# Optimization experiments

Measured on AMD Instinct MI355X. Metric: run time of the kernel, lower is better.

The kernel has to match this reference:

```python
import jax, jax.numpy as jnp
import numpy as np
from math import sqrt

B = 128        # graphs
P = 256        # nodes per graph
N = B * P      # total nodes
E = 524288     # edges (avg degree 16)
S = 32         # seed queries per graph
DQ = DK = DV = 128
H = 4          # heads


def setup_inputs() -> dict:
    key = jax.random.key(0)
    ks = jax.random.split(key, 10)
    Q = jax.random.normal(ks[0], (B, S, DQ), dtype=jnp.float32)
    x = jax.random.normal(ks[1], (N, DK), dtype=jnp.float32)
    # edges constrained within each graph block of P nodes
    src = jax.random.randint(ks[2], (E,), 0, N)
    dst = (src // P) * P + jax.random.randint(ks[3], (E,), 0, P)
    edge_index = jnp.stack([src, dst]).astype(jnp.int64)
    batch = (jnp.arange(N) // P).astype(jnp.int64)
    s = 1.0 / sqrt(DV)
    Wq = jax.random.normal(ks[4], (DQ, DV), dtype=jnp.float32) * s
    Wk = jax.random.normal(ks[5], (DK, DV), dtype=jnp.float32) * s
    Wv = jax.random.normal(ks[6], (DK, DV), dtype=jnp.float32) * s
    Wo = jax.random.normal(ks[7], (DV, DV), dtype=jnp.float32) * s
    z = jnp.zeros((DV,), jnp.float32)
    o = jnp.ones((DV,), jnp.float32)
    return {"Q": Q, "x": x, "edge_index": edge_index, "batch": batch,
            "Wq": Wq, "bq": z, "Wk": Wk, "bk": z, "Wv": Wv, "bv": z,
            "Wo": Wo, "bo": z, "g0": o, "b0": z, "g1": o, "b1": z}


def _gcn(x, edge_index, W, b):
    # PyG GCNConv: self-loops + symmetric deg^-1/2 normalization, then scatter-add
    xw = x @ W                                   # [N, DV]
    row, col = edge_index[0], edge_index[1]
    deg = jnp.zeros((N,), xw.dtype).at[col].add(1.0) + 1.0  # +1 for self-loop
    dinv = jax.lax.rsqrt(deg)
    coef = dinv[row] * dinv[col]                 # [E]
    out = jnp.zeros_like(xw).at[col].add(xw[row] * coef[:, None])
    out = out + xw * (dinv * dinv)[:, None]      # self-loop messages
    return out + b


def _ln(x, g, b, eps=1e-5):
    mu = x.mean(-1, keepdims=True)
    var = ((x - mu) ** 2).mean(-1, keepdims=True)
    return (x - mu) * jax.lax.rsqrt(var + eps) * g + b


def reference(Q, x, edge_index, batch, Wq, bq, Wk, bk, Wv, bv, Wo, bo, g0, b0, g1, b1):
    dh = DV // H
    Qp = Q @ Wq + bq                             # [B, S, DV]
    K = _gcn(x, edge_index, Wk, bk)              # [N, DV]
    V = _gcn(x, edge_index, Wv, bv)
    # to_dense_batch: equal-size graphs -> static reshape; mask all valid
    Kd = K.reshape(B, P, DV)
    Vd = V.reshape(B, P, DV)
    mask = jnp.ones((B, P), Qp.dtype)
    mask_add = (1.0 - mask) * -1e9               # [B, P]
    # split heads on last dim (== torch split(dim=2) + cat(dim=0))
    Qh = Qp.reshape(B, S, H, dh)
    Kh = Kd.reshape(B, P, H, dh)
    Vh = Vd.reshape(B, P, H, dh)
    scores = jnp.einsum('bshd,bphd->bhsp', Qh, Kh) / sqrt(DV)
    A = jax.nn.softmax(scores + mask_add[:, None, None, :], axis=-1)
    Oh = Qh + jnp.einsum('bhsp,bphd->bshd', A, Vh)
    O = Oh.reshape(B, S, DV)
    O = _ln(O, g0, b0)
    O = O + jax.nn.relu(O @ Wo + bo)
    O = _ln(O, g1, b1)
    return O
```

## Files before the change

### kernel.cpp

```cpp
#include <hip/hip_runtime.h>

typedef unsigned int uint32;
typedef unsigned short ushort;
typedef __attribute__((ext_vector_type(8))) short short8;
typedef __attribute__((ext_vector_type(4))) float f32x4;

#define NNODES 32768
#define NGRAPH 128
#define PNODES 256
#define SQ 32
#define NEDGE 524288
#define DIM 128
#define NHEAD 4
#define MAXDEG 64

__device__ __forceinline__ float u2f(uint32 u){ union{uint32 i; float f;} c; c.i=u; return c.f; }
__device__ __forceinline__ uint32 f2bf(float f){
  union{float f; uint32 i;} c; c.f=f;
  return (c.i + 0x7FFFu + ((c.i>>16)&1u)) >> 16;
}
__device__ __forceinline__ uint32 pk2(float a, float b){ return f2bf(a) | (f2bf(b)<<16); }

__global__ __launch_bounds__(256) void k_prep0(const float* __restrict__ Wk,
    const float* __restrict__ Wv, const float* __restrict__ Wq, const float* __restrict__ Wo,
    ushort* __restrict__ WTk, ushort* __restrict__ WTv, ushort* __restrict__ WTq,
    ushort* __restrict__ WTo, int4* __restrict__ zbase){
  const int bid = blockIdx.x;
  const int t = threadIdx.x;
  if (bid >= 4){
    int idx = (bid-4)*256 + t;
    if (idx < 8192) zbase[idx] = int4{0,0,0,0};
    return;
  }
  __shared__ __align__(16) float Ws2[128*132];
  const float* W = (bid==0) ? Wk : (bid==1) ? Wv : (bid==2) ? Wq : Wo;
  ushort* WT     = (bid==0) ? WTk : (bid==1) ? WTv : (bid==2) ? WTq : WTo;
  for (int idx = t; idx < 4096; idx += 256){
    int k = idx >> 5, c4 = idx & 31;
    *(float4*)&Ws2[k*132 + c4*4] = *(const float4*)&W[k*128 + c4*4];
  }
  __syncthreads();
  for (int idx = t; idx < 2048; idx += 256){
    int n = idx & 127, c8 = idx >> 7;
    uint4 p;
    p.x = pk2(Ws2[(c8*8+0)*132 + n], Ws2[(c8*8+1)*132 + n]);
    p.y = pk2(Ws2[(c8*8+2)*132 + n], Ws2[(c8*8+3)*132 + n]);
    p.z = pk2(Ws2[(c8*8+4)*132 + n], Ws2[(c8*8+5)*132 + n]);
    p.w = pk2(Ws2[(c8*8+6)*132 + n], Ws2[(c8*8+7)*132 + n]);
    *(uint4*)&WT[n*128 + c8*8] = p;
  }
}

__global__ void k_edges(const int* __restrict__ ei, int* __restrict__ deg,
                        ushort* __restrict__ ebuf){
  int e = blockIdx.x*256 + threadIdx.x;
  int s = ei[e];
  int d = ei[NEDGE + e];
  int i = atomicAdd(&deg[d], 1);
  if (i < MAXDEG) ebuf[(d << 6) + i] = (ushort)(s & 255);
}

#define APITCH 132
__global__ __launch_bounds__(512) void k_aggkv(
    const int* __restrict__ deg, const ushort* __restrict__ ebuf,
    const float* __restrict__ x,
    const ushort* __restrict__ WTk, const float* __restrict__ bk, ushort* __restrict__ Kb,
    const ushort* __restrict__ WTv, const float* __restrict__ bv, ushort* __restrict__ VbT)
{
  __shared__ __align__(16) char lds[138240];
  uint32* A    = (uint32*)lds;
  ushort* Au   = (ushort*)lds;
  ushort* xT   = (ushort*)(lds + 67584);
  ushort* xa_s = (ushort*)(lds + 67584);
  ushort* wtA  = (ushort*)(lds + 102400);
  ushort* wtB  = (ushort*)(lds + 0);
  ushort* KK   = (ushort*)(lds + 67584);
  ushort* VVt  = (ushort*)(lds + 102400);
  float*  dvs  = (float*)(lds + 137216);
  const int t = threadIdx.x;
  const int g = blockIdx.x >> 1, half = blockIdx.x & 1;
  const int base = g*PNODES;
  const int rbase = half*128;

  if (t < 256) dvs[t] = rsqrtf((float)(deg[base + t] + 1));
  {
    uint4* Az = (uint4*)A;
    for (int i = t; i < 4224; i += 512) Az[i] = uint4{0,0,0,0};
  }
  __syncthreads();
  if (t < 128){
    float dn = dvs[rbase + t];
    int src = rbase + t;
    uint32 nb = f2bf(dn*dn);
    A[t*APITCH + (src>>1)] = (src & 1) ? (nb<<16) : nb;
  }
  for (int idx = t; idx < 8192; idx += 512){
    int f = idx & 127, s4 = idx >> 7;
    const int r = base + s4*4;
    float v0 = x[(r+0)*DIM + f];
    float v1 = x[(r+1)*DIM + f];
    float v2 = x[(r+2)*DIM + f];
    float v3 = x[(r+3)*DIM + f];
    uint2 p; p.x = pk2(v0, v1); p.y = pk2(v2, v3);
    *(uint2*)&xT[f*264 + s4*4] = p;
  }
  __syncthreads();
  {
    const int r = t >> 2, sub = t & 3;
    const int n = base + rbase + r;
    const int dg = min(deg[n], MAXDEG);
    const float dn = dvs[rbase + r];
    const ushort* eb = ebuf + (n << 6);
    for (int i = 0; i < dg; ++i){
      const int srcl = eb[i];
      if (((srcl >> 1) & 3) != sub) continue;
      const float coef = dn * dvs[srcl];
      uint32* cell = &A[r*APITCH + (srcl>>1)];
      uint32 old = *cell;
      if (srcl & 1){
        float cur = u2f(old & 0xffff0000u);
        *cell = (old & 0xffffu) | (f2bf(cur + coef) << 16);
      } else {
        float cur = u2f(old << 16);
        *cell = (old & 0xffff0000u) | f2bf(cur + coef);
      }
    }
  }
  __syncthreads();
  const int lane = t & 63, w = t >> 6;
  const int r16 = lane & 15, kg = lane >> 4;
  f32x4 acc[8];
  #pragma unroll
  for (int j = 0; j < 8; ++j) acc[j] = (f32x4){0.f,0.f,0.f,0.f};
  #pragma unroll
  for (int kc = 0; kc < 8; ++kc){
    const short8 a = *(const short8*)&Au[(w*16 + r16)*264 + kc*32 + kg*8];
    #pragma unroll
    for (int ct = 0; ct < 8; ++ct){
      const short8 b = *(const short8*)&xT[(ct*16 + r16)*264 + kc*32 + kg*8];
      acc[ct] = __builtin_amdgcn_mfma_f32_16x16x32_bf16(a, b, acc[ct], 0, 0, 0);
    }
  }
  __syncthreads();
  #pragma unroll
  for (int ct = 0; ct < 8; ++ct)
    #pragma unroll
    for (int q = 0; q < 4; ++q)
      xa_s[(w*16 + kg*4 + q)*136 + ct*16 + r16] = (ushort)f2bf(acc[ct][q]);
  for (int idx = t; idx < 2048; idx += 512){
    int n = idx >> 4, c8 = idx & 15;
    *(uint4*)&wtA[n*136 + c8*8] = *(const uint4*)&WTk[n*128 + c8*8];
    *(uint4*)&wtB[n*136 + c8*8] = *(const uint4*)&WTv[n*128 + c8*8];
  }
  __syncthreads();
  f32x4 k0[8], v0[8];
  #pragma unroll
  for (int j = 0; j < 8; ++j){ k0[j] = (f32x4){0.f,0.f,0.f,0.f}; v0[j] = (f32x4){0.f,0.f,0.f,0.f}; }
  #pragma unroll
  for (int kc = 0; kc < 4; ++kc){
    const short8 a = *(const short8*)&xa_s[(w*16 + r16)*136 + kc*32 + kg*8];
    #pragma unroll
    for (int ct = 0; ct < 8; ++ct){
      const short8 b0 = *(const short8*)&wtA[(ct*16 + r16)*136 + kc*32 + kg*8];
      const short8 b1 = *(const short8*)&wtB[(ct*16 + r16)*136 + kc*32 + kg*8];
      k0[ct] = __builtin_amdgcn_mfma_f32_16x16x32_bf16(a, b0, k0[ct], 0, 0, 0);
      v0[ct] = __builtin_amdgcn_mfma_f32_16x16x32_bf16(a, b1, v0[ct], 0, 0, 0);
    }
  }
  __syncthreads();
  #pragma unroll
  for (int ct = 0; ct < 8; ++ct){
    const int col = ct*16 + r16;
    const float bkc = bk[col], bvc = bv[col];
    #pragma unroll
    for (int q = 0; q < 4; ++q){
      const int r = w*16 + kg*4 + q;
      KK[r*136 + col]  = (ushort)f2bf(k0[ct][q] + bkc);
      VVt[col*136 + r] = (ushort)f2bf(v0[ct][q] + bvc);
    }
  }
  __syncthreads();
  for (int idx = t; idx < 2048; idx += 512){
    int r = idx >> 4, c8 = idx & 15;
    *(uint4*)&Kb[(base + rbase + r)*DIM + c8*8] = *(const uint4*)&KK[r*136 + c8*8];
  }
  for (int idx = t; idx < 2048; idx += 512){
    int d = idx >> 4, c8 = idx & 15;
    *(uint4*)&VbT[(g*128 + d)*PNODES + rbase + c8*8] = *(const uint4*)&VVt[d*136 + c8*8];
  }
}

__global__ __launch_bounds__(512) void k_attnepi(
    const float* __restrict__ Qin, const ushort* __restrict__ WTq,
    const float* __restrict__ bq,
    const ushort* __restrict__ Kb, const ushort* __restrict__ VbT,
    const ushort* __restrict__ WoT, const float* __restrict__ bo,
    const float* __restrict__ g0, const float* __restrict__ b0,
    const float* __restrict__ g1, const float* __restrict__ b1,
    float* __restrict__ out)
{
  __shared__ __align__(16) char lds[151040];
  ushort* KbS = (ushort*)lds;
  ushort* VT  = (ushort*)lds;
  ushort* R2  = (ushort*)(lds + 69632);
  float*  S   = (float*)(lds + 104448);
  float*  Zf  = (float*)(lds + 104448);
  ushort* Pb  = (ushort*)(lds + 121344);
  float*  Yf  = (float*)(lds + 121344);
  float*  Ob  = (float*)(lds + 129792);
  float*  Qres= (float*)(lds + 138240);
  ushort* Qb  = (ushort*)(lds + 146688);

  const int t = threadIdx.x;
  const int w = t >> 6, lane = t & 63;
  const int r16 = lane & 15, kg = lane >> 4;
  const int g = blockIdx.x >> 1, qh = blockIdx.x & 1;
  const int qr0 = g*SQ + qh*16;

  for (int idx = t; idx < 4096; idx += 512){
    int r = idx >> 4, c8 = idx & 15;
    *(uint4*)&KbS[r*136 + c8*8] = *(const uint4*)&Kb[(g*256 + r)*128 + c8*8];
  }
  for (int idx = t; idx < 2048; idx += 512){
    int n = idx >> 4, c8 = idx & 15;
    *(uint4*)&R2[n*136 + c8*8] = *(const uint4*)&WTq[n*128 + c8*8];
  }
  short8 qin[4];
  #pragma unroll
  for (int kc = 0; kc < 4; ++kc){
    const float4 f0 = *(const float4*)&Qin[(qr0 + r16)*128 + kc*32 + kg*8];
    const float4 f1 = *(const float4*)&Qin[(qr0 + r16)*128 + kc*32 + kg*8 + 4];
    union { short8 s; uint32 u[4]; } c;
    c.u[0] = pk2(f0.x, f0.y); c.u[1] = pk2(f0.z, f0.w);
    c.u[2] = pk2(f1.x, f1.y); c.u[3] = pk2(f1.z, f1.w);
    qin[kc] = c.s;
  }
  __syncthreads();

  {
    f32x4 qa = (f32x4){0.f,0.f,0.f,0.f};
    #pragma unroll
    for (int kc = 0; kc < 4; ++kc){
      const short8 bf = *(const short8*)&R2[(w*16 + r16)*136 + kc*32 + kg*8];
      qa = __builtin_amdgcn_mfma_f32_16x16x32_bf16(qin[kc], bf, qa, 0, 0, 0);
    }
    #pragma unroll
    for (int q = 0; q < 4; ++q){
      const int row = kg*4 + q, col = w*16 + r16;
      const float v = qa[q] + bq[col];
      Qres[row*132 + col] = v;
      Qb[row*136 + col] = (ushort)f2bf(v);
    }
  }
  __syncthreads();

  {
    short8 qf[4];
    #pragma unroll
    for (int kc = 0; kc < 4; ++kc)
      qf[kc] = *(const short8*)&Qb[r16*136 + kc*32 + kg*8];
    f32x4 sa[2];
    sa[0] = (f32x4){0.f,0.f,0.f,0.f}; sa[1] = (f32x4){0.f,0.f,0.f,0.f};
    #pragma unroll
    for (int kc = 0; kc < 4; ++kc){
      #pragma unroll
      for (int nt = 0; nt < 2; ++nt){
        const short8 bf = *(const short8*)&KbS[((w*2+nt)*16 + r16)*136 + kc*32 + kg*8];
        sa[nt] = __builtin_amdgcn_mfma_f32_16x16x32_bf16(qf[kc], bf, sa[nt], 0, 0, 0);
      }
    }
    #pragma unroll
    for (int nt = 0; nt < 2; ++nt)
      #pragma unroll
      for (int q = 0; q < 4; ++q)
        S[(kg*4+q)*264 + (w*2+nt)*16 + r16] = sa[nt][q] * 0.08838834764831845f;
  }
  __syncthreads();

  {
    const int row = t >> 5, j = t & 31;
    float vals[8];
    float m = -1e30f;
    #pragma unroll
    for (int u = 0; u < 8; ++u){
      vals[u] = S[row*264 + j + 32*u];
      m = fmaxf(m, vals[u]);
    }
    m = fmaxf(m, __shfl_xor(m, 1));
    m = fmaxf(m, __shfl_xor(m, 2));
    m = fmaxf(m, __shfl_xor(m, 4));
    m = fmaxf(m, __shfl_xor(m, 8));
    m = fmaxf(m, __shfl_xor(m, 16));
    float sum = 0.f;
    #pragma unroll
    for (int u = 0; u < 8; ++u){
      vals[u] = __expf(vals[u] - m);
      sum += vals[u];
    }
    sum += __shfl_xor(sum, 1);
    sum += __shfl_xor(sum, 2);
    sum += __shfl_xor(sum, 4);
    sum += __shfl_xor(sum, 8);
    sum += __shfl_xor(sum, 16);
    float inv = 1.f / sum;
    #pragma unroll
    for (int u = 0; u < 8; ++u)
      Pb[row*264 + j + 32*u] = (ushort)f2bf(vals[u] * inv);
  }
  for (int idx = t; idx < 4096; idx += 512){
    int d = idx >> 5, c8 = idx & 31;
    *(uint4*)&VT[d*264 + c8*8] = *(const uint4*)&VbT[(g*128 + d)*PNODES + c8*8];
  }
  __syncthreads();

  {
    f32x4 oa = (f32x4){0.f,0.f,0.f,0.f};
    #pragma unroll
    for (int kc = 0; kc < 8; ++kc){
      const short8 pa = *(const short8*)&Pb[r16*264 + kc*32 + kg*8];
      const short8 vb = *(const short8*)&VT[(w*16 + r16)*264 + kc*32 + kg*8];
      oa = __builtin_amdgcn_mfma_f32_16x16x32_bf16(pa, vb, oa, 0, 0, 0);
    }
    #pragma unroll
    for (int q = 0; q < 4; ++q){
      const int row = kg*4 + q, col = w*16 + r16;
      Ob[row*132 + col] = oa[q] + Qres[row*132 + col];
    }
  }
  __syncthreads();

  #pragma unroll
  for (int rr = 0; rr < 2; ++rr){
    const int row = w*2 + rr;
    float x0 = Ob[row*132 + 2*lane], x1 = Ob[row*132 + 2*lane + 1];
    float s = x0 + x1;
    s += __shfl_xor(s,1); s += __shfl_xor(s,2); s += __shfl_xor(s,4);
    s += __shfl_xor(s,8); s += __shfl_xor(s,16); s += __shfl_xor(s,32);
    float mu = s * 0.0078125f;
    float d0 = x0 - mu, d1 = x1 - mu;
    float vv = d0*d0 + d1*d1;
    vv += __shfl_xor(vv,1); vv += __shfl_xor(vv,2); vv += __shfl_xor(vv,4);
    vv += __shfl_xor(vv,8); vv += __shfl_xor(vv,16); vv += __shfl_xor(vv,32);
    float rs = rsqrtf(vv*0.0078125f + 1e-5f);
    const float2 gv = *(const float2*)&g0[2*lane];
    const float2 bv = *(const float2*)&b0[2*lane];
    float y0 = d0*rs*gv.x + bv.x;
    float y1 = d1*rs*gv.y + bv.y;
    Yf[row*132 + 2*lane] = y0; Yf[row*132 + 2*lane + 1] = y1;
    *(uint32*)&Qb[row*136 + 2*lane] = pk2(y0, y1);
  }
  for (int idx = t; idx < 2048; idx += 512){
    int n = idx >> 4, c8 = idx & 15;
    *(uint4*)&R2[n*136 + c8*8] = *(const uint4*)&WoT[n*128 + c8*8];
  }
  __syncthreads();

  {
    f32x4 fa = (f32x4){0.f,0.f,0.f,0.f};
    #pragma unroll
    for (int kc = 0; kc < 4; ++kc){
      const short8 ya = *(const short8*)&Qb[r16*136 + kc*32 + kg*8];
      const short8 wb = *(const short8*)&R2[(w*16 + r16)*136 + kc*32 + kg*8];
      fa = __builtin_amdgcn_mfma_f32_16x16x32_bf16(ya, wb, fa, 0, 0, 0);
    }
    #pragma unroll
    for (int q = 0; q < 4; ++q){
      const int row = kg*4 + q, col = w*16 + r16;
      Zf[row*132 + col] = Yf[row*132 + col] + fmaxf(fa[q] + bo[col], 0.f);
    }
  }
  __syncthreads();

  #pragma unroll
  for (int rr = 0; rr < 2; ++rr){
    const int row = w*2 + rr;
    float z0 = Zf[row*132 + 2*lane], z1 = Zf[row*132 + 2*lane + 1];
    float s = z0 + z1;
    s += __shfl_xor(s,1); s += __shfl_xor(s,2); s += __shfl_xor(s,4);
    s += __shfl_xor(s,8); s += __shfl_xor(s,16); s += __shfl_xor(s,32);
    float mu = s * 0.0078125f;
    float d0 = z0 - mu, d1 = z1 - mu;
    float vv = d0*d0 + d1*d1;
    vv += __shfl_xor(vv,1); vv += __shfl_xor(vv,2); vv += __shfl_xor(vv,4);
    vv += __shfl_xor(vv,8); vv += __shfl_xor(vv,16); vv += __shfl_xor(vv,32);
    float rs = rsqrtf(vv*0.0078125f + 1e-5f);
    const float2 g1v = *(const float2*)&g1[2*lane];
    const float2 b1v = *(const float2*)&b1[2*lane];
    float2 o;
    o.x = d0*rs*g1v.x + b1v.x;
    o.y = d1*rs*g1v.y + b1v.y;
    *(float2*)&out[(qr0 + row)*128 + 2*lane] = o;
  }
}

extern "C" void kernel_launch(void* const* d_in, const int* in_sizes, int n_in,
                              void* d_out, int out_size, void* d_ws, size_t ws_size,
                              hipStream_t stream){
  const float* Q   = (const float*)d_in[0];
  const float* x   = (const float*)d_in[1];
  const int*   ei  = (const int*)d_in[2];
  const float* Wq  = (const float*)d_in[4];
  const float* bq  = (const float*)d_in[5];
  const float* Wk  = (const float*)d_in[6];
  const float* bk  = (const float*)d_in[7];
  const float* Wv  = (const float*)d_in[8];
  const float* bv  = (const float*)d_in[9];
  const float* Wo  = (const float*)d_in[10];
  const float* bo  = (const float*)d_in[11];
  const float* g0  = (const float*)d_in[12];
  const float* b0  = (const float*)d_in[13];
  const float* g1  = (const float*)d_in[14];
  const float* b1  = (const float*)d_in[15];

  char* ws = (char*)d_ws;
  ushort* Kb   = (ushort*)(ws);
  ushort* VbT  = (ushort*)(ws + 8388608);
  ushort* WTk  = (ushort*)(ws + 16777216);
  ushort* WTv  = (ushort*)(ws + 16809984);
  ushort* WTq  = (ushort*)(ws + 16842752);
  ushort* WTo  = (ushort*)(ws + 16875520);
  int*    deg  = (int*)(ws + 16908288);
  ushort* ebuf = (ushort*)(ws + 17039360);

  k_prep0<<<36, 256, 0, stream>>>(Wk, Wv, Wq, Wo, WTk, WTv, WTq, WTo, (int4*)deg);
  k_edges<<<NEDGE/256, 256, 0, stream>>>(ei, deg, ebuf);
  k_aggkv<<<NGRAPH*2, 512, 0, stream>>>(deg, ebuf, x, WTk, bk, Kb, WTv, bv, VbT);
  k_attnepi<<<NGRAPH*2, 512, 0, stream>>>(Q, WTq, bq, Kb, VbT, WTo, bo, g0, b0, g1, b1, (float*)d_out);
}
```

Baseline: 73.78 us.

## Prefetch weights, K and V tiles into registers early to overlap global loads

In the GCN kernel, the Wk/Wv transposed tiles are loaded into registers at kernel start and written to LDS later, hiding their global latency behind the adjacency build and aggregation GEMM. The self-loop diagonal write is moved after the first barrier so one __syncthreads can be dropped; it now does a read-modify-write so it keeps the other packed half. In the attention kernel, Wq, Q, K, V and Wo are all issued as register prefetches up front and stored to LDS at the stage where each is needed. This raises register pressure considerably, which may reduce occupancy or cause spills.

```diff
diff --git a/kernel.cpp b/kernel.cpp
--- a/kernel.cpp
+++ b/kernel.cpp
@@ -82,17 +82,19 @@
   const int base = g*PNODES;
   const int rbase = half*128;
 
+  uint4 wAr[4], wBr[4];
+  #pragma unroll
+  for (int i = 0; i < 4; ++i){
+    const int idx = t + i*512;
+    const int n = idx >> 4, c8 = idx & 15;
+    wAr[i] = *(const uint4*)&WTk[n*128 + c8*8];
+    wBr[i] = *(const uint4*)&WTv[n*128 + c8*8];
+  }
+
   if (t < 256) dvs[t] = rsqrtf((float)(deg[base + t] + 1));
   {
     uint4* Az = (uint4*)A;
     for (int i = t; i < 4224; i += 512) Az[i] = uint4{0,0,0,0};
-  }
-  __syncthreads();
-  if (t < 128){
-    float dn = dvs[rbase + t];
-    int src = rbase + t;
-    uint32 nb = f2bf(dn*dn);
-    A[t*APITCH + (src>>1)] = (src & 1) ? (nb<<16) : nb;
   }
   for (int idx = t; idx < 8192; idx += 512){
     int f = idx & 127, s4 = idx >> 7;
@@ -105,6 +107,14 @@
     *(uint2*)&xT[f*264 + s4*4] = p;
   }
   __syncthreads();
+  if (t < 128){
+    float dn = dvs[rbase + t];
+    int src = rbase + t;
+    uint32 nb = f2bf(dn*dn);
+    uint32 old = A[t*APITCH + (src>>1)];
+    A[t*APITCH + (src>>1)] = (src & 1) ? ((old & 0xffffu) | (nb<<16))
+                                       : ((old & 0xffff0000u) | nb);
+  }
   {
     const int r = t >> 2, sub = t & 3;
     const int n = base + rbase + r;
@@ -147,10 +157,12 @@
     #pragma unroll
     for (int q = 0; q < 4; ++q)
       xa_s[(w*16 + kg*4 + q)*136 + ct*16 + r16] = (ushort)f2bf(acc[ct][q]);
-  for (int idx = t; idx < 2048; idx += 512){
-    int n = idx >> 4, c8 = idx & 15;
-    *(uint4*)&wtA[n*136 + c8*8] = *(const uint4*)&WTk[n*128 + c8*8];
-    *(uint4*)&wtB[n*136 + c8*8] = *(const uint4*)&WTv[n*128 + c8*8];
+  #pragma unroll
+  for (int i = 0; i < 4; ++i){
+    const int idx = t + i*512;
+    const int n = idx >> 4, c8 = idx & 15;
+    *(uint4*)&wtA[n*136 + c8*8] = wAr[i];
+    *(uint4*)&wtB[n*136 + c8*8] = wBr[i];
   }
   __syncthreads();
   f32x4 k0[8], v0[8];
@@ -217,22 +229,42 @@
   const int g = blockIdx.x >> 1, qh = blockIdx.x & 1;
   const int qr0 = g*SQ + qh*16;
 
-  for (int idx = t; idx < 4096; idx += 512){
-    int r = idx >> 4, c8 = idx & 15;
-    *(uint4*)&KbS[r*136 + c8*8] = *(const uint4*)&Kb[(g*256 + r)*128 + c8*8];
-  }
-  for (int idx = t; idx < 2048; idx += 512){
-    int n = idx >> 4, c8 = idx & 15;
-    *(uint4*)&R2[n*136 + c8*8] = *(const uint4*)&WTq[n*128 + c8*8];
+  uint4 wq[4];
+  #pragma unroll
+  for (int i = 0; i < 4; ++i){
+    const int idx = t + i*512;
+    wq[i] = *(const uint4*)&WTq[(idx >> 4)*128 + (idx & 15)*8];
+  }
+  float4 qf0[4], qf1[4];
+  #pragma unroll
+  for (int kc = 0; kc < 4; ++kc){
+    qf0[kc] = *(const float4*)&Qin[(qr0 + r16)*128 + kc*32 + kg*8];
+    qf1[kc] = *(const float4*)&Qin[(qr0 + r16)*128 + kc*32 + kg*8 + 4];
+  }
+  uint4 kr[8];
+  #pragma unroll
+  for (int i = 0; i < 8; ++i){
+    const int idx = t + i*512;
+    kr[i] = *(const uint4*)&Kb[(g*256 + (idx >> 4))*128 + (idx & 15)*8];
+  }
+  uint4 vr[8];
+  #pragma unroll
+  for (int i = 0; i < 8; ++i){
+    const int idx = t + i*512;
+    vr[i] = *(const uint4*)&VbT[(g*128 + (idx >> 5))*PNODES + (idx & 31)*8];
+  }
+
+  #pragma unroll
+  for (int i = 0; i < 4; ++i){
+    const int idx = t + i*512;
+    *(uint4*)&R2[(idx >> 4)*136 + (idx & 15)*8] = wq[i];
   }
   short8 qin[4];
   #pragma unroll
   for (int kc = 0; kc < 4; ++kc){
-    const float4 f0 = *(const float4*)&Qin[(qr0 + r16)*128 + kc*32 + kg*8];
-    const float4 f1 = *(const float4*)&Qin[(qr0 + r16)*128 + kc*32 + kg*8 + 4];
     union { short8 s; uint32 u[4]; } c;
-    c.u[0] = pk2(f0.x, f0.y); c.u[1] = pk2(f0.z, f0.w);
-    c.u[2] = pk2(f1.x, f1.y); c.u[3] = pk2(f1.z, f1.w);
+    c.u[0] = pk2(qf0[kc].x, qf0[kc].y); c.u[1] = pk2(qf0[kc].z, qf0[kc].w);
+    c.u[2] = pk2(qf1[kc].x, qf1[kc].y); c.u[3] = pk2(qf1[kc].z, qf1[kc].w);
     qin[kc] = c.s;
   }
   __syncthreads();
@@ -243,6 +275,11 @@
     for (int kc = 0; kc < 4; ++kc){
       const short8 bf = *(const short8*)&R2[(w*16 + r16)*136 + kc*32 + kg*8];
       qa = __builtin_amdgcn_mfma_f32_16x16x32_bf16(qin[kc], bf, qa, 0, 0, 0);
+    }
+    #pragma unroll
+    for (int i = 0; i < 8; ++i){
+      const int idx = t + i*512;
+      *(uint4*)&KbS[(idx >> 4)*136 + (idx & 15)*8] = kr[i];
     }
     #pragma unroll
     for (int q = 0; q < 4; ++q){
@@ -255,10 +292,10 @@
   __syncthreads();
 
   {
-    short8 qf[4];
+    short8 qfr[4];
     #pragma unroll
     for (int kc = 0; kc < 4; ++kc)
-      qf[kc] = *(const short8*)&Qb[r16*136 + kc*32 + kg*8];
+      qfr[kc] = *(const short8*)&Qb[r16*136 + kc*32 + kg*8];
     f32x4 sa[2];
     sa[0] = (f32x4){0.f,0.f,0.f,0.f}; sa[1] = (f32x4){0.f,0.f,0.f,0.f};
     #pragma unroll
@@ -266,7 +303,7 @@
       #pragma unroll
       for (int nt = 0; nt < 2; ++nt){
         const short8 bf = *(const short8*)&KbS[((w*2+nt)*16 + r16)*136 + kc*32 + kg*8];
-        sa[nt] = __builtin_amdgcn_mfma_f32_16x16x32_bf16(qf[kc], bf, sa[nt], 0, 0, 0);
+        sa[nt] = __builtin_amdgcn_mfma_f32_16x16x32_bf16(qfr[kc], bf, sa[nt], 0, 0, 0);
       }
     }
     #pragma unroll
@@ -277,6 +314,12 @@
   }
   __syncthreads();
 
+  uint4 wo[4];
+  #pragma unroll
+  for (int i = 0; i < 4; ++i){
+    const int idx = t + i*512;
+    wo[i] = *(const uint4*)&WoT[(idx >> 4)*128 + (idx & 15)*8];
+  }
   {
     const int row = t >> 5, j = t & 31;
     float vals[8];
@@ -307,9 +350,10 @@
     for (int u = 0; u < 8; ++u)
       Pb[row*264 + j + 32*u] = (ushort)f2bf(vals[u] * inv);
   }
-  for (int idx = t; idx < 4096; idx += 512){
-    int d = idx >> 5, c8 = idx & 31;
-    *(uint4*)&VT[d*264 + c8*8] = *(const uint4*)&VbT[(g*128 + d)*PNODES + c8*8];
+  #pragma unroll
+  for (int i = 0; i < 8; ++i){
+    const int idx = t + i*512;
+    *(uint4*)&VT[(idx >> 5)*264 + (idx & 31)*8] = vr[i];
   }
   __syncthreads();
 
@@ -349,9 +393,10 @@
     Yf[row*132 + 2*lane] = y0; Yf[row*132 + 2*lane + 1] = y1;
     *(uint32*)&Qb[row*136 + 2*lane] = pk2(y0, y1);
   }
-  for (int idx = t; idx < 2048; idx += 512){
-    int n = idx >> 4, c8 = idx & 15;
-    *(uint4*)&R2[n*136 + c8*8] = *(const uint4*)&WoT[n*128 + c8*8];
+  #pragma unroll
+  for (int i = 0; i < 4; ++i){
+    const int idx = t + i*512;
+    *(uint4*)&R2[(idx >> 4)*136 + (idx & 15)*8] = wo[i];
   }
   __syncthreads();
 
```

New measurement: 88.69 us. +20.2%, slower.
